# Kernel tuning notes

Hardware: AMD Instinct MI355X
Metric: run time of the kernel (lower is better)

## Reference

```python
import jax, jax.numpy as jnp
import numpy as np

WS = 7          # window size (square)
SHIFT = 3       # shift size
NH = 8          # num heads
DIM = 256
B, H, W = 32, 56, 56


def _relative_position_index(ws: int) -> np.ndarray:
    coords = np.stack(np.meshgrid(np.arange(ws), np.arange(ws), indexing='ij'))  # (2, ws, ws)
    cf = coords.reshape(2, -1)                                                   # (2, N)
    rel = cf[:, :, None] - cf[:, None, :]                                        # (2, N, N)
    rel = rel.transpose(1, 2, 0).copy()
    rel[:, :, 0] += ws - 1
    rel[:, :, 1] += ws - 1
    rel[:, :, 0] *= 2 * ws - 1
    return rel.sum(-1).reshape(-1).astype(np.int32)                              # (N*N,)


def _shift_mask(h: int, w: int, ws: int, shift: int) -> np.ndarray:
    img = np.zeros((h, w), dtype=np.float32)
    cnt = 0
    for hs in ((0, -ws), (-ws, -shift), (-shift, None)):
        for wsl in ((0, -ws), (-ws, -shift), (-shift, None)):
            img[hs[0]:hs[1], wsl[0]:wsl[1]] = cnt
            cnt += 1
    nwh, nww = h // ws, w // ws
    m = img.reshape(nwh, ws, nww, ws).transpose(0, 2, 1, 3).reshape(nwh * nww, ws * ws)
    am = m[:, None, :] - m[:, :, None]                 # (nW, N, N)
    return np.where(am != 0, np.float32(-100.0), np.float32(0.0))


def setup_inputs() -> dict:
    key = jax.random.key(0)
    ks = jax.random.split(key, 5)
    x = jax.random.normal(ks[0], (B, H, W, DIM), jnp.float32)
    qkv_weight = jax.random.normal(ks[1], (3 * DIM, DIM), jnp.float32) * 0.02
    qkv_bias = jnp.zeros((3 * DIM,), jnp.float32)
    proj_weight = jax.random.normal(ks[2], (DIM, DIM), jnp.float32) * 0.02
    proj_bias = jnp.zeros((DIM,), jnp.float32)
    rel_bias_table = jax.random.normal(ks[3], ((2 * WS - 1) ** 2, NH), jnp.float32) * 0.02
    rel_pos_index = jnp.asarray(_relative_position_index(WS))
    return {
        'x': x, 'qkv_weight': qkv_weight, 'qkv_bias': qkv_bias,
        'proj_weight': proj_weight, 'proj_bias': proj_bias,
        'rel_bias_table': rel_bias_table, 'rel_pos_index': rel_pos_index,
    }


def reference(x, qkv_weight, qkv_bias, proj_weight, proj_bias, rel_bias_table, rel_pos_index):
    b, h, w, c = x.shape
    n = WS * WS
    hd = c // NH
    nwh, nww = h // WS, w // WS
    nw = nwh * nww

    # relative position bias: (1, NH, N, N)
    bias = rel_bias_table[rel_pos_index].reshape(n, n, NH).transpose(2, 0, 1)[None]

    # cyclic shift
    xs = jnp.roll(x, (-SHIFT, -SHIFT), axis=(1, 2))

    # window partition -> (B*nW, N, C)
    xw = xs.reshape(b, nwh, WS, nww, WS, c).transpose(0, 1, 3, 2, 4, 5).reshape(b * nw, n, c)

    qkv = xw @ qkv_weight.T + qkv_bias
    qkv = qkv.reshape(b * nw, n, 3, NH, hd).transpose(2, 0, 3, 1, 4)  # (3, B*nW, NH, N, hd)
    q = qkv[0] * (hd ** -0.5)
    k = qkv[1]
    v = qkv[2]

    attn = jnp.einsum('bhnd,bhmd->bhnm', q, k) + bias                # (B*nW, NH, N, N)

    # shift mask (static)
    amask = jnp.asarray(_shift_mask(h, w, WS, SHIFT))                # (nW, N, N)
    attn = attn.reshape(b, nw, NH, n, n) + amask[None, :, None]
    attn = jax.nn.softmax(attn.reshape(b * nw, NH, n, n), axis=-1)

    out = jnp.einsum('bhnm,bhmd->bhnd', attn, v)                     # (B*nW, NH, N, hd)
    out = out.transpose(0, 2, 1, 3).reshape(b * nw, n, c)
    out = out @ proj_weight.T + proj_bias

    # window reverse + reverse shift
    out = out.reshape(b, nwh, nww, WS, WS, c).transpose(0, 1, 3, 2, 4, 5).reshape(b, h, w, c)
    out = jnp.roll(out, (SHIFT, SHIFT), axis=(1, 2))
    return out
```

## Files before the change

kernel.cpp:

```cpp
#include <hip/hip_runtime.h>
#include <hip/hip_bf16.h>


#define NTOK 49
#define DIM_ 256
#define NH_  8
#define NQKV 196608
#define NPRJ 65536
#define NTAB1 19208
#define NTAB4 (4 * NTAB1)

#define WSP_B  393216ull
#define TAB_B  524288ull
#define Q_B    831744ull
#define QK_EL  25690112
#define Q_BYTES 51380224ull
#define K_B    (Q_B + Q_BYTES)
#define VT_B   (K_B + Q_BYTES)
#define VT_BYTES 58720256ull
#define NEED_BIG (VT_B + VT_BYTES)
#define NEED_TAB (TAB_B + (unsigned long long)NTAB4 * 4)

typedef short v8s __attribute__((ext_vector_type(8)));
typedef float v4f __attribute__((ext_vector_type(4)));

#define MFMA16 __builtin_amdgcn_mfma_f32_16x16x32_bf16
#define LGKM_WAIT() asm volatile("s_waitcnt lgkmcnt(0)" ::: "memory")

static __device__ __forceinline__ v8s zero_v8s() {
    v8s z = {0, 0, 0, 0, 0, 0, 0, 0};
    return z;
}

static __device__ __forceinline__ v8s lds_frag(const __hip_bfloat16* p, int row,
                                               int stride, int koff, int nrows) {
    if (row < nrows) return *(const v8s*)(p + row * stride + koff);
    return zero_v8s();
}

static __device__ __forceinline__ v8s cvt8(const float* p) {
    v4f a = *(const v4f*)p;
    v4f b = *(const v4f*)(p + 4);
    union { v8s v; __hip_bfloat16 h[8]; } r;
    r.h[0] = __float2bfloat16(a[0]); r.h[1] = __float2bfloat16(a[1]);
    r.h[2] = __float2bfloat16(a[2]); r.h[3] = __float2bfloat16(a[3]);
    r.h[4] = __float2bfloat16(b[0]); r.h[5] = __float2bfloat16(b[1]);
    r.h[6] = __float2bfloat16(b[2]); r.h[7] = __float2bfloat16(b[3]);
    return r.v;
}

__global__ __launch_bounds__(256) void prep_kernel(
    const float* __restrict__ qkvW, const float* __restrict__ projW,
    const float* __restrict__ rbt, const int* __restrict__ rpi,
    __hip_bfloat16* __restrict__ wsQ, __hip_bfloat16* __restrict__ wsP,
    float* __restrict__ tab4, int doTab)
{
    int i = blockIdx.x * 256 + threadIdx.x;
    if (i < NQKV) { wsQ[i] = __float2bfloat16(qkvW[i]); return; }
    int j = i - NQKV;
    if (j < NPRJ) { wsP[j] = __float2bfloat16(projW[j]); return; }
    int t = j - NPRJ;
    if (!doTab || t >= NTAB4) return;
    int cls = t / NTAB1, rem = t - cls * NTAB1;
    int h = rem / 2401, p = rem - h * 2401;
    int row = p / 49, col = p - row * 49;
    int rh = (cls & 1) ? (((row / 7) < 4) ? 1 : 2) : 0;
    int rw = (cls & 2) ? (((row % 7) < 4) ? 1 : 2) : 0;
    int ch = (cls & 1) ? (((col / 7) < 4) ? 1 : 2) : 0;
    int cw = (cls & 2) ? (((col % 7) < 4) ? 1 : 2) : 0;
    float mask = ((rh * 3 + rw) != (ch * 3 + cw)) ? -100.0f : 0.0f;
    tab4[t] = rbt[rpi[p] * NH_ + h] + mask;
}

__global__ __launch_bounds__(256) void qkv_kernel(
    const float* __restrict__ x,
    const float* __restrict__ qkvB,
    const __hip_bfloat16* __restrict__ wsQ,
    __hip_bfloat16* __restrict__ Q,
    __hip_bfloat16* __restrict__ K,
    __hip_bfloat16* __restrict__ VT)
{
    constexpr int SXS = 264;
    __shared__ alignas(16) __hip_bfloat16 s_x[NTOK * SXS];

    const int tid = threadIdx.x, wave = tid >> 6, lane = tid & 63;
    const int quad = lane >> 4, l16 = lane & 15;
    const int win = blockIdx.x;
    const int b = win >> 6, wh = (win >> 3) & 7, wwi = win & 7;

    for (int i = tid; i < NTOK * 64; i += 256) {
        int tok = i >> 6, f4 = (i & 63) * 4;
        int r = tok / 7, c = tok - r * 7;
        int hg = wh * 7 + r + 3; if (hg >= 56) hg -= 56;
        int wg = wwi * 7 + c + 3; if (wg >= 56) wg -= 56;
        float4 v = *(const float4*)(x + ((b * 56 + hg) * 56 + wg) * DIM_ + f4);
        __hip_bfloat16* dst = s_x + tok * SXS + f4;
        dst[0] = __float2bfloat16(v.x);
        dst[1] = __float2bfloat16(v.y);
        dst[2] = __float2bfloat16(v.z);
        dst[3] = __float2bfloat16(v.w);
    }
    for (int i = tid; i < 256 * 7; i += 256) {
        int fg = i / 7, col = 49 + (i - fg * 7);
        int h = fg >> 5, feat = fg & 31;
        VT[((win * NH_ + h) * 32 + feat) * 56 + col] = __float2bfloat16(0.0f);
    }
    __syncthreads();

    const float qscale = 0.17677669529663687f;

    for (int t = 0; t < 12; ++t) {
        int ntb = (wave * 12 + t) * 16;
        int nout = ntb + l16;
        const __hip_bfloat16* wrow = wsQ + nout * DIM_;
        v8s B[8];
        #pragma unroll
        for (int ks = 0; ks < 8; ++ks)
            B[ks] = *(const v8s*)(wrow + ks * 32 + quad * 8);
        float bias = qkvB[nout];
        int mat = ntb >> 8;
        int h = (ntb >> 5) & 7;
        int colb = ntb & 16;
        #pragma unroll
        for (int mt = 0; mt < 4; ++mt) {
            v4f acc = {0.f, 0.f, 0.f, 0.f};
            #pragma unroll
            for (int ks = 0; ks < 8; ++ks) {
                v8s a = lds_frag(s_x, mt * 16 + l16, SXS, ks * 32 + quad * 8, NTOK);
                acc = MFMA16(a, B[ks], acc, 0, 0, 0);
            }
            #pragma unroll
            for (int rg = 0; rg < 4; ++rg) {
                int tok = mt * 16 + quad * 4 + rg;
                if (tok < NTOK) {
                    float val = acc[rg] + bias;
                    if (mat == 0)
                        Q[((win * NH_ + h) * NTOK + tok) * 32 + colb + l16] =
                            __float2bfloat16(val * qscale);
                    else if (mat == 1)
                        K[((win * NH_ + h) * NTOK + tok) * 32 + colb + l16] =
                            __float2bfloat16(val);
                    else
                        VT[((win * NH_ + h) * 32 + colb + l16) * 56 + tok] =
                            __float2bfloat16(val);
                }
            }
        }
    }
}

__global__ __launch_bounds__(256) void attn_kernel(
    const float* __restrict__ tab4,
    const __hip_bfloat16* __restrict__ K,
    const __hip_bfloat16* __restrict__ VT,
    __hip_bfloat16* __restrict__ Q)
{
    constexpr int PS = 72;
    __shared__ alignas(16) __hip_bfloat16 s_p[4][NTOK * PS];

    const int tid = threadIdx.x, wave = tid >> 6, lane = tid & 63;
    const int quad = lane >> 4, l16 = lane & 15;
    const int id = blockIdx.x * 4 + wave;
    const int win = id >> 3, h = id & 7;
    const int wh = (win >> 3) & 7, wwi = win & 7;
    const int cls = ((wh == 7) ? 1 : 0) | ((wwi == 7) ? 2 : 0);
    const float* tabh = tab4 + (cls * NH_ + h) * 2401;
    __hip_bfloat16* qs = Q + (win * NH_ + h) * (NTOK * 32);
    const __hip_bfloat16* ks_ = K + (win * NH_ + h) * (NTOK * 32);
    const __hip_bfloat16* vts = VT + (win * NH_ + h) * (32 * 56);
    __hip_bfloat16* wp = s_p[wave];

    v8s qa[4], kb[4];
    #pragma unroll
    for (int mt = 0; mt < 4; ++mt) {
        int tok = mt * 16 + l16;
        qa[mt] = *(const v8s*)(qs + tok * 32 + quad * 8);
        kb[mt] = *(const v8s*)(ks_ + tok * 32 + quad * 8);
    }
    v8s pb[2][2];
    #pragma unroll
    for (int nt = 0; nt < 2; ++nt) {
        const __hip_bfloat16* vr = vts + (nt * 16 + l16) * 56;
        pb[nt][0] = *(const v8s*)(vr + quad * 8);
        pb[nt][1] = (quad == 3) ? zero_v8s() : *(const v8s*)(vr + 32 + quad * 8);
    }

    #pragma unroll
    for (int mtile = 0; mtile < 4; ++mtile) {
        v4f sa[4];
        #pragma unroll
        for (int nt = 0; nt < 4; ++nt) {
            v4f z = {0.f, 0.f, 0.f, 0.f};
            sa[nt] = MFMA16(qa[mtile], kb[nt], z, 0, 0, 0);
        }
        #pragma unroll
        for (int rg = 0; rg < 4; ++rg) {
            int row = mtile * 16 + quad * 4 + rg;
            bool rok = row < NTOK;
            float v[4];
            float rmax = -1e30f;
            #pragma unroll
            for (int nt = 0; nt < 4; ++nt) {
                int col = nt * 16 + l16;
                float s = -1e30f;
                if (rok && col < NTOK)
                    s = sa[nt][rg] + tabh[row * 49 + col];
                v[nt] = s;
                rmax = fmaxf(rmax, s);
            }
            #pragma unroll
            for (int mm = 8; mm >= 1; mm >>= 1)
                rmax = fmaxf(rmax, __shfl_xor(rmax, mm, 64));
            float rsum = 0.f;
            #pragma unroll
            for (int nt = 0; nt < 4; ++nt) {
                float e = (v[nt] <= -1e29f) ? 0.f : __expf(v[nt] - rmax);
                v[nt] = e;
                rsum += e;
            }
            #pragma unroll
            for (int mm = 8; mm >= 1; mm >>= 1)
                rsum += __shfl_xor(rsum, mm, 64);
            if (rok) {
                float inv = 1.0f / rsum;
                #pragma unroll
                for (int nt = 0; nt < 4; ++nt)
                    wp[row * PS + nt * 16 + l16] = __float2bfloat16(v[nt] * inv);
            }
        }
    }
    LGKM_WAIT();

    #pragma unroll
    for (int mtile = 0; mtile < 4; ++mtile) {
        v8s pa0 = lds_frag(wp, mtile * 16 + l16, PS, quad * 8, NTOK);
        v8s pa1 = lds_frag(wp, mtile * 16 + l16, PS, 32 + quad * 8, NTOK);
        #pragma unroll
        for (int nt = 0; nt < 2; ++nt) {
            v4f z = {0.f, 0.f, 0.f, 0.f};
            v4f acc = MFMA16(pa0, pb[nt][0], z, 0, 0, 0);
            acc = MFMA16(pa1, pb[nt][1], acc, 0, 0, 0);
            #pragma unroll
            for (int rg = 0; rg < 4; ++rg) {
                int tok = mtile * 16 + quad * 4 + rg;
                if (tok < NTOK)
                    qs[tok * 32 + nt * 16 + l16] = __float2bfloat16(acc[rg]);
            }
        }
    }
}

__global__ __launch_bounds__(256) void proj_kernel(
    const __hip_bfloat16* __restrict__ OH,
    const __hip_bfloat16* __restrict__ wsP,
    const float* __restrict__ projB,
    float* __restrict__ out)
{
    const int tid = threadIdx.x, wave = tid >> 6, lane = tid & 63;
    const int quad = lane >> 4, l16 = lane & 15;
    const int win = blockIdx.x;
    const int b = win >> 6, wh = (win >> 3) & 7, wwi = win & 7;
    const int m0 = wave * 16;

    const __hip_bfloat16* ohw = OH + (size_t)win * (NH_ * NTOK * 32);
    v8s af[8];
    int tokA = m0 + l16;
    #pragma unroll
    for (int ks = 0; ks < 8; ++ks)
        af[ks] = (tokA < NTOK)
                   ? *(const v8s*)(ohw + ks * (NTOK * 32) + tokA * 32 + quad * 8)
                   : zero_v8s();

    int ooff[4];
    #pragma unroll
    for (int rg = 0; rg < 4; ++rg) {
        int row = m0 + quad * 4 + rg;
        if (row < NTOK) {
            int r = row / 7, c = row - r * 7;
            int hg = wh * 7 + r + 3; if (hg >= 56) hg -= 56;
            int wg = wwi * 7 + c + 3; if (wg >= 56) wg -= 56;
            ooff[rg] = ((b * 56 + hg) * 56 + wg) * DIM_;
        } else ooff[rg] = -1;
    }

    #pragma unroll
    for (int t = 0; t < 16; ++t) {
        const __hip_bfloat16* wrow = wsP + (t * 16 + l16) * DIM_;
        v4f acc = {0.f, 0.f, 0.f, 0.f};
        #pragma unroll
        for (int ks = 0; ks < 8; ++ks) {
            v8s bfr = *(const v8s*)(wrow + ks * 32 + quad * 8);
            acc = MFMA16(af[ks], bfr, acc, 0, 0, 0);
        }
        float pbv = projB[t * 16 + l16];
        #pragma unroll
        for (int rg = 0; rg < 4; ++rg)
            if (ooff[rg] >= 0)
                out[ooff[rg] + t * 16 + l16] = acc[rg] + pbv;
    }
}

__global__ __launch_bounds__(256, 2) void swin_attn_fused(
    const float* __restrict__ x,
    const float* __restrict__ qkvB,
    const float* __restrict__ projB,
    const float* __restrict__ rbt,
    const int*   __restrict__ rpi,
    const __hip_bfloat16* __restrict__ wsQ,
    const __hip_bfloat16* __restrict__ wsP,
    const float* __restrict__ biasTab,
    float*       __restrict__ out)
{
    constexpr int QKS = 40;
    constexpr int VTS = 72;
    constexpr int PS  = 72;
    constexpr int OS  = 264;
    constexpr int WVSZ = 6224;

    __shared__ alignas(16) __hip_bfloat16 s_wv[4 * WVSZ];
    __shared__ alignas(16) __hip_bfloat16 s_o[NTOK * OS];
    __shared__ int s_off[NTOK];
    __shared__ int s_reg[NTOK];

    const int tid  = threadIdx.x;
    const int wave = tid >> 6;
    const int lane = tid & 63;
    const int quad = lane >> 4;
    const int l16  = lane & 15;

    const int wid  = blockIdx.x;
    const int b    = wid >> 6;
    const int wIdx = wid & 63;
    const int wh   = wIdx >> 3;
    const int wwi  = wIdx & 7;

    if (tid < NTOK) {
        int r = tid / 7, c = tid - r * 7;
        int hs = wh * 7 + r, ws = wwi * 7 + c;
        int hg = hs + 3; if (hg >= 56) hg -= 56;
        int wg = ws + 3; if (wg >= 56) wg -= 56;
        s_off[tid] = ((b * 56 + hg) * 56 + wg) * DIM_;
        int rh = (hs < 49) ? 0 : ((hs < 53) ? 1 : 2);
        int rw = (ws < 49) ? 0 : ((ws < 53) ? 1 : 2);
        s_reg[tid] = rh * 3 + rw;
    }

    __hip_bfloat16* wq  = s_wv + wave * WVSZ;
    __hip_bfloat16* wk  = wq + NTOK * QKS;
    __hip_bfloat16* wvt = wq + 2 * NTOK * QKS;
    __hip_bfloat16* wp  = wq;

    for (int i = lane; i < 32 * 15; i += 64) {
        int f = i / 15, kk = 49 + (i % 15);
        wvt[f * VTS + kk] = __float2bfloat16(0.0f);
    }
    __syncthreads();

    const float qscale = 0.17677669529663687f;

    v4f pacc_unused; (void)pacc_unused;

    for (int hp = 0; hp < 2; ++hp) {
        const int h = wave * 2 + hp;
        LGKM_WAIT();

        for (int mh = 0; mh < 2; ++mh) {
            const int mbase = mh * 32;
            v8s at[2][8];
            #pragma unroll
            for (int sub = 0; sub < 2; ++sub) {
                int tok = mbase + sub * 16 + l16;
                const float* xr = (tok < NTOK) ? (x + s_off[tok]) : nullptr;
                #pragma unroll
                for (int ks = 0; ks < 8; ++ks)
                    at[sub][ks] = xr ? cvt8(xr + ks * 32 + quad * 8) : zero_v8s();
            }
            #pragma unroll
            for (int t = 0; t < 6; ++t) {
                int mat = t >> 1, ntile = t & 1;
                int nout = mat * 256 + h * 32 + ntile * 16 + l16;
                const __hip_bfloat16* wrow = wsQ + nout * DIM_;
                v4f a0 = {0.f, 0.f, 0.f, 0.f}, a1 = {0.f, 0.f, 0.f, 0.f};
                #pragma unroll
                for (int ks = 0; ks < 8; ++ks) {
                    v8s bfr = *(const v8s*)(wrow + ks * 32 + quad * 8);
                    a0 = MFMA16(at[0][ks], bfr, a0, 0, 0, 0);
                    a1 = MFMA16(at[1][ks], bfr, a1, 0, 0, 0);
                }
                float bias  = qkvB[nout];
                float scale = (mat == 0) ? qscale : 1.0f;
                #pragma unroll
                for (int sub = 0; sub < 2; ++sub) {
                    v4f acc = sub ? a1 : a0;
                    #pragma unroll
                    for (int rg = 0; rg < 4; ++rg) {
                        int row = mbase + sub * 16 + quad * 4 + rg;
                        if (row < NTOK) {
                            float val = (acc[rg] + bias) * scale;
                            int col = ntile * 16 + l16;
                            __hip_bfloat16 bv = __float2bfloat16(val);
                            if (mat == 0)      wq[row * QKS + col] = bv;
                            else if (mat == 1) wk[row * QKS + col] = bv;
                            else               wvt[col * VTS + row] = bv;
                        }
                    }
                }
            }
        }
        LGKM_WAIT();

        v8s qa[4], kb[4];
        #pragma unroll
        for (int i = 0; i < 4; ++i) {
            qa[i] = lds_frag(wq, i * 16 + l16, QKS, quad * 8, NTOK);
            kb[i] = lds_frag(wk, i * 16 + l16, QKS, quad * 8, NTOK);
        }
        int regc[4];
        #pragma unroll
        for (int nt = 0; nt < 4; ++nt) {
            int col = nt * 16 + l16;
            regc[nt] = (col < NTOK) ? s_reg[col] : -1;
        }
        LGKM_WAIT();
        const float* tabh = biasTab ? (biasTab + h * 2401) : nullptr;
        #pragma unroll
        for (int mtile = 0; mtile < 4; ++mtile) {
            v4f sa[4];
            #pragma unroll
            for (int nt = 0; nt < 4; ++nt) {
                v4f z = {0.f, 0.f, 0.f, 0.f};
                sa[nt] = MFMA16(qa[mtile], kb[nt], z, 0, 0, 0);
            }
            #pragma unroll
            for (int rg = 0; rg < 4; ++rg) {
                int row = mtile * 16 + quad * 4 + rg;
                bool rok = row < NTOK;
                int rr = rok ? s_reg[row] : -2;
                float v[4];
                float rmax = -1e30f;
                #pragma unroll
                for (int nt = 0; nt < 4; ++nt) {
                    int col = nt * 16 + l16;
                    float s = -1e30f;
                    if (rok && col < NTOK) {
                        float bv = tabh ? tabh[row * 49 + col]
                                        : rbt[rpi[row * 49 + col] * NH_ + h];
                        s = sa[nt][rg] + bv;
                        if (rr != regc[nt]) s -= 100.0f;
                    }
                    v[nt] = s;
                    rmax = fmaxf(rmax, s);
                }
                #pragma unroll
                for (int mm = 8; mm >= 1; mm >>= 1)
                    rmax = fmaxf(rmax, __shfl_xor(rmax, mm, 64));
                float rsum = 0.f;
                #pragma unroll
                for (int nt = 0; nt < 4; ++nt) {
                    float e = (v[nt] <= -1e29f) ? 0.f : __expf(v[nt] - rmax);
                    v[nt] = e;
                    rsum += e;
                }
                #pragma unroll
                for (int mm = 8; mm >= 1; mm >>= 1)
                    rsum += __shfl_xor(rsum, mm, 64);
                if (rok) {
                    float inv = 1.0f / rsum;
                    #pragma unroll
                    for (int nt = 0; nt < 4; ++nt)
                        wp[row * PS + nt * 16 + l16] = __float2bfloat16(v[nt] * inv);
                }
            }
        }
        LGKM_WAIT();

        v8s pb[2][2];
        #pragma unroll
        for (int nt = 0; nt < 2; ++nt)
            #pragma unroll
            for (int ks = 0; ks < 2; ++ks)
                pb[nt][ks] = *(const v8s*)(wvt + (nt * 16 + l16) * VTS + ks * 32 + quad * 8);
        #pragma unroll
        for (int mtile = 0; mtile < 4; ++mtile) {
            v8s pa0 = lds_frag(wp, mtile * 16 + l16, PS, quad * 8, NTOK);
            v8s pa1 = lds_frag(wp, mtile * 16 + l16, PS, 32 + quad * 8, NTOK);
            #pragma unroll
            for (int nt = 0; nt < 2; ++nt) {
                v4f z = {0.f, 0.f, 0.f, 0.f};
                v4f acc = MFMA16(pa0, pb[nt][0], z, 0, 0, 0);
                acc = MFMA16(pa1, pb[nt][1], acc, 0, 0, 0);
                #pragma unroll
                for (int rg = 0; rg < 4; ++rg) {
                    int row = mtile * 16 + quad * 4 + rg;
                    if (row < NTOK)
                        s_o[row * OS + h * 32 + nt * 16 + l16] = __float2bfloat16(acc[rg]);
                }
            }
        }
    }
    __syncthreads();

    {
        int m0 = wave * 16;
        v8s af[8];
        #pragma unroll
        for (int ks = 0; ks < 8; ++ks)
            af[ks] = lds_frag(s_o, m0 + l16, OS, ks * 32 + quad * 8, NTOK);
        #pragma unroll
        for (int t = 0; t < 16; ++t) {
            const __hip_bfloat16* wrow = wsP + (t * 16 + l16) * DIM_;
            v4f acc = {0.f, 0.f, 0.f, 0.f};
            #pragma unroll
            for (int ks = 0; ks < 8; ++ks) {
                v8s bfr = *(const v8s*)(wrow + ks * 32 + quad * 8);
                acc = MFMA16(af[ks], bfr, acc, 0, 0, 0);
            }
            float pbv = projB[t * 16 + l16];
            #pragma unroll
            for (int rg = 0; rg < 4; ++rg) {
                int row = m0 + quad * 4 + rg;
                if (row < NTOK)
                    out[s_off[row] + t * 16 + l16] = acc[rg] + pbv;
            }
        }
    }
}

extern "C" void kernel_launch(void* const* d_in, const int* in_sizes, int n_in,
                              void* d_out, int out_size, void* d_ws, size_t ws_size,
                              hipStream_t stream) {
    const float* x     = (const float*)d_in[0];
    const float* qkvW  = (const float*)d_in[1];
    const float* qkvB  = (const float*)d_in[2];
    const float* projW = (const float*)d_in[3];
    const float* projB = (const float*)d_in[4];
    const float* rbt   = (const float*)d_in[5];
    const int*   rpi   = (const int*)d_in[6];
    float* o = (float*)d_out;

    __hip_bfloat16* wsQ = (__hip_bfloat16*)d_ws;
    __hip_bfloat16* wsP = (__hip_bfloat16*)((char*)d_ws + WSP_B);
    float* tab4         = (float*)((char*)d_ws + TAB_B);
    __hip_bfloat16* Q   = (__hip_bfloat16*)((char*)d_ws + Q_B);
    __hip_bfloat16* K   = (__hip_bfloat16*)((char*)d_ws + K_B);
    __hip_bfloat16* VT  = (__hip_bfloat16*)((char*)d_ws + VT_B);

    const int prepBlocks = (NQKV + NPRJ + NTAB4 + 255) / 256;

    if (ws_size >= NEED_BIG) {
        prep_kernel<<<prepBlocks, 256, 0, stream>>>(qkvW, projW, rbt, rpi,
                                                    wsQ, wsP, tab4, 1);
        qkv_kernel<<<2048, 256, 0, stream>>>(x, qkvB, wsQ, Q, K, VT);
        attn_kernel<<<4096, 256, 0, stream>>>(tab4, K, VT, Q);
        proj_kernel<<<2048, 256, 0, stream>>>(Q, wsP, projB, o);
    } else {
        int doTab = (ws_size >= NEED_TAB) ? 1 : 0;
        prep_kernel<<<prepBlocks, 256, 0, stream>>>(qkvW, projW, rbt, rpi,
                                                    wsQ, wsP, tab4, doTab);
        swin_attn_fused<<<2048, 256, 0, stream>>>(x, qkvB, projB, rbt, rpi,
                                                  wsQ, wsP, doTab ? tab4 : nullptr, o);
    }
}
```

Before: 497.9 us.

## Retile QKV projection onto 32x32x16 MFMA with a transposed V computation

The QKV projection kernel moves from 16x16x32 MFMA tiles to 32x32x16 MFMA tiles. Each wave now handles 32 output columns and two 32-token row tiles, so every weight fragment load is shared by two MFMAs. For the V part the operands are swapped so the result comes out with features in rows, which makes the VT stores contiguous along tokens. Launch bounds now request 4 blocks per CU. The trade-off is higher register pressure from the 16-wide accumulators, and one tile wastes work on padded rows past token 49. Whether this kernel runs by default is unclear, since a separate fused kernel appears to exist.

```diff
diff --git a/kernel.cpp b/kernel.cpp
--- a/kernel.cpp
+++ b/kernel.cpp
@@ -23,12 +23,21 @@
 
 typedef short v8s __attribute__((ext_vector_type(8)));
 typedef float v4f __attribute__((ext_vector_type(4)));
+typedef float v16f __attribute__((ext_vector_type(16)));
 
 #define MFMA16 __builtin_amdgcn_mfma_f32_16x16x32_bf16
+#define MFMA32 __builtin_amdgcn_mfma_f32_32x32x16_bf16
 #define LGKM_WAIT() asm volatile("s_waitcnt lgkmcnt(0)" ::: "memory")
 
 static __device__ __forceinline__ v8s zero_v8s() {
     v8s z = {0, 0, 0, 0, 0, 0, 0, 0};
+    return z;
+}
+
+static __device__ __forceinline__ v16f zero_v16f() {
+    v16f z;
+    #pragma unroll
+    for (int i = 0; i < 16; ++i) z[i] = 0.0f;
     return z;
 }
 
@@ -72,7 +81,7 @@
     tab4[t] = rbt[rpi[p] * NH_ + h] + mask;
 }
 
-__global__ __launch_bounds__(256) void qkv_kernel(
+__global__ __launch_bounds__(256, 4) void qkv_kernel(
     const float* __restrict__ x,
     const float* __restrict__ qkvB,
     const __hip_bfloat16* __restrict__ wsQ,
@@ -84,7 +93,7 @@
     __shared__ alignas(16) __hip_bfloat16 s_x[NTOK * SXS];
 
     const int tid = threadIdx.x, wave = tid >> 6, lane = tid & 63;
-    const int quad = lane >> 4, l16 = lane & 15;
+    const int l32 = lane & 31, half = lane >> 5;
     const int win = blockIdx.x;
     const int b = win >> 6, wh = (win >> 3) & 7, wwi = win & 7;
 
@@ -108,42 +117,68 @@
     __syncthreads();
 
     const float qscale = 0.17677669529663687f;
-
-    for (int t = 0; t < 12; ++t) {
-        int ntb = (wave * 12 + t) * 16;
-        int nout = ntb + l16;
-        const __hip_bfloat16* wrow = wsQ + nout * DIM_;
-        v8s B[8];
-        #pragma unroll
-        for (int ks = 0; ks < 8; ++ks)
-            B[ks] = *(const v8s*)(wrow + ks * 32 + quad * 8);
-        float bias = qkvB[nout];
-        int mat = ntb >> 8;
-        int h = (ntb >> 5) & 7;
-        int colb = ntb & 16;
-        #pragma unroll
-        for (int mt = 0; mt < 4; ++mt) {
-            v4f acc = {0.f, 0.f, 0.f, 0.f};
-            #pragma unroll
-            for (int ks = 0; ks < 8; ++ks) {
-                v8s a = lds_frag(s_x, mt * 16 + l16, SXS, ks * 32 + quad * 8, NTOK);
-                acc = MFMA16(a, B[ks], acc, 0, 0, 0);
-            }
-            #pragma unroll
-            for (int rg = 0; rg < 4; ++rg) {
-                int tok = mt * 16 + quad * 4 + rg;
-                if (tok < NTOK) {
-                    float val = acc[rg] + bias;
-                    if (mat == 0)
-                        Q[((win * NH_ + h) * NTOK + tok) * 32 + colb + l16] =
-                            __float2bfloat16(val * qscale);
-                    else if (mat == 1)
-                        K[((win * NH_ + h) * NTOK + tok) * 32 + colb + l16] =
-                            __float2bfloat16(val);
-                    else
-                        VT[((win * NH_ + h) * 32 + colb + l16) * 56 + tok] =
-                            __float2bfloat16(val);
-                }
+    const int r1 = (32 + l32 < NTOK) ? (32 + l32) : 0;
+
+    for (int t = 0; t < 6; ++t) {
+        const int nb = (wave * 6 + t) * 32;
+        const int mat = nb >> 8;
+        const int h = (nb >> 5) & 7;
+        const __hip_bfloat16* wrow  = wsQ + (nb + l32) * DIM_ + half * 8;
+        const __hip_bfloat16* arow0 = s_x + l32 * SXS + half * 8;
+        const __hip_bfloat16* arow1 = s_x + r1 * SXS + half * 8;
+
+        v16f acc0 = zero_v16f(), acc1 = zero_v16f();
+
+        if (mat < 2) {
+            #pragma unroll
+            for (int kh = 0; kh < 2; ++kh) {
+                v8s wf[8];
+                #pragma unroll
+                for (int k = 0; k < 8; ++k)
+                    wf[k] = *(const v8s*)(wrow + kh * 128 + k * 16);
+                #pragma unroll
+                for (int k = 0; k < 8; ++k) {
+                    v8s a0 = *(const v8s*)(arow0 + kh * 128 + k * 16);
+                    v8s a1 = *(const v8s*)(arow1 + kh * 128 + k * 16);
+                    acc0 = MFMA32(a0, wf[k], acc0, 0, 0, 0);
+                    acc1 = MFMA32(a1, wf[k], acc1, 0, 0, 0);
+                }
+            }
+            float bias = qkvB[nb + l32];
+            float sc = (mat == 0) ? qscale : 1.0f;
+            __hip_bfloat16* dst = (mat == 0 ? Q : K) + (win * NH_ + h) * (NTOK * 32) + l32;
+            #pragma unroll
+            for (int rg = 0; rg < 16; ++rg) {
+                int rowoff = (rg & 3) + 8 * (rg >> 2) + 4 * half;
+                dst[rowoff * 32] = __float2bfloat16((acc0[rg] + bias) * sc);
+                int tok1 = 32 + rowoff;
+                if (tok1 < NTOK)
+                    dst[tok1 * 32] = __float2bfloat16((acc1[rg] + bias) * sc);
+            }
+        } else {
+            #pragma unroll
+            for (int kh = 0; kh < 2; ++kh) {
+                v8s wf[8];
+                #pragma unroll
+                for (int k = 0; k < 8; ++k)
+                    wf[k] = *(const v8s*)(wrow + kh * 128 + k * 16);
+                #pragma unroll
+                for (int k = 0; k < 8; ++k) {
+                    v8s b0 = *(const v8s*)(arow0 + kh * 128 + k * 16);
+                    v8s b1 = *(const v8s*)(arow1 + kh * 128 + k * 16);
+                    acc0 = MFMA32(wf[k], b0, acc0, 0, 0, 0);
+                    acc1 = MFMA32(wf[k], b1, acc1, 0, 0, 0);
+                }
+            }
+            __hip_bfloat16* dst = VT + (win * NH_ + h) * (32 * 56);
+            const int tok1 = 32 + l32;
+            #pragma unroll
+            for (int rg = 0; rg < 16; ++rg) {
+                int feat = (rg & 3) + 8 * (rg >> 2) + 4 * half;
+                float bias = qkvB[nb + feat];
+                dst[feat * 56 + l32] = __float2bfloat16(acc0[rg] + bias);
+                if (tok1 < NTOK)
+                    dst[feat * 56 + tok1] = __float2bfloat16(acc1[rg] + bias);
             }
         }
     }
@@ -358,8 +393,6 @@
 
     const float qscale = 0.17677669529663687f;
 
-    v4f pacc_unused; (void)pacc_unused;
-
     for (int hp = 0; hp < 2; ++hp) {
         const int h = wave * 2 + hp;
         LGKM_WAIT();
```

New measurement: 503.5 us. No clear change (+1.1%).
